# Performance work log

Measured on AMD Instinct MI355X. Metric: run time of the kernel, lower is better.

## Reference

```python
import jax, jax.numpy as jnp
import numpy as np

NUM_CLASSES = 80
INPUT_SHAPE = (416.0, 416.0)
ANCHORS_MASK0 = np.array([6, 7, 8])
CONF_THRES = 0.5
NMS_THRES = 0.4
IMAGE_SHAPE = (416.0, 416.0)
MAX_DET = 100          # fixed-size padded NMS output (jit-compatible)
CLASS_OFFSET = 4096.0  # class-aware box offset == independent per-class NMS
NEG = jnp.float32(-1e9)


def setup_inputs() -> dict:
    key = jax.random.key(0)
    inputs_1 = jax.random.normal(key, (32, 255, 52, 52), dtype=jnp.float32)
    anchors = jnp.array([[10, 13], [16, 30], [33, 23], [30, 61], [62, 45],
                         [59, 119], [116, 90], [156, 198], [373, 326]], dtype=jnp.float32)
    return {"inputs_1": inputs_1, "anchors": anchors}


def _decode(inputs_1, anchors):
    B, C, H, W = inputs_1.shape
    A = len(ANCHORS_MASK0)
    attrs = C // A  # 5 + num_classes
    # [B, A, H, W, attrs]
    pred = inputs_1.reshape(B, A, attrs, H, W).transpose(0, 1, 3, 4, 2)
    xy = jax.nn.sigmoid(pred[..., 0:2])
    wh = pred[..., 2:4]
    conf = jax.nn.sigmoid(pred[..., 4])
    cls = jax.nn.sigmoid(pred[..., 5:])
    stride_h = INPUT_SHAPE[0] / H
    stride_w = INPUT_SHAPE[1] / W
    anc = anchors[ANCHORS_MASK0] / jnp.array([stride_w, stride_h], jnp.float32)  # [A,2]
    gx = jnp.arange(W, dtype=jnp.float32)
    gy = jnp.arange(H, dtype=jnp.float32)
    bx = xy[..., 0] + gx[None, None, None, :]
    by = xy[..., 1] + gy[None, None, :, None]
    bw = jnp.exp(wh[..., 0]) * anc[:, 0][None, :, None, None]
    bh = jnp.exp(wh[..., 1]) * anc[:, 1][None, :, None, None]
    boxes = jnp.stack([bx, by, bw, bh], -1) / jnp.array([W, H, W, H], jnp.float32)
    return jnp.concatenate([boxes.reshape(B, -1, 4),
                            conf.reshape(B, -1, 1),
                            cls.reshape(B, -1, NUM_CLASSES)], axis=-1)  # [B, A*H*W, 5+C]


def _iou(box, boxes):
    lt = jnp.maximum(box[:2], boxes[:, :2])
    rb = jnp.minimum(box[2:], boxes[:, 2:])
    wh = jnp.clip(rb - lt, 0.0)
    inter = wh[:, 0] * wh[:, 1]
    a1 = (box[2] - box[0]) * (box[3] - box[1])
    a2 = (boxes[:, 2] - boxes[:, 0]) * (boxes[:, 3] - boxes[:, 1])
    return inter / (a1 + a2 - inter + 1e-9)


def _nms(pred0):
    # pred0: [N, 5+C] (image 0, matching torch code which only processes prediction[0])
    cx, cy, w, h = pred0[:, 0], pred0[:, 1], pred0[:, 2], pred0[:, 3]
    corners = jnp.stack([cx - w / 2, cy - h / 2, cx + w / 2, cy + h / 2], -1)  # [N,4]
    class_conf = jnp.max(pred0[:, 5:], axis=1)
    class_pred = jnp.argmax(pred0[:, 5:], axis=1)
    score = pred0[:, 4] * class_conf  # obj_conf * class_conf, same score nms() receives
    valid = score >= CONF_THRES
    # offsetting boxes by class id makes a single NMS pass equivalent to the per-class loop
    obox = corners + (class_pred.astype(jnp.float32) * CLASS_OFFSET)[:, None]
    s0 = jnp.where(valid, score, NEG)

    def step(scores, _):
        i = jnp.argmax(scores)
        flag = scores[i] > NEG / 2
        iou = _iou(obox[i], obox)
        new_scores = jnp.where(iou > NMS_THRES, NEG, scores).at[i].set(NEG)
        return new_scores, (i, flag)

    _, (idxs, flags) = jax.lax.scan(step, s0, None, length=MAX_DET)
    det = jnp.concatenate([
        corners[idxs],                                  # x1,y1,x2,y2
        pred0[idxs, 4:5],                               # obj conf
        class_conf[idxs][:, None],                      # class conf
        class_pred[idxs].astype(jnp.float32)[:, None],  # class id
    ], axis=1)  # [MAX_DET, 7]
    # yolo_correct_boxes: xywh -> yx min/max scaled to image_shape
    box_xy = (det[:, 0:2] + det[:, 2:4]) / 2.0
    box_wh = det[:, 2:4] - det[:, 0:2]
    box_yx = box_xy[:, ::-1]
    box_hw = box_wh[:, ::-1]
    mins = box_yx - box_hw / 2.0
    maxes = box_yx + box_hw / 2.0
    scale = jnp.array([IMAGE_SHAPE[0], IMAGE_SHAPE[1], IMAGE_SHAPE[0], IMAGE_SHAPE[1]], jnp.float32)
    boxes_corr = jnp.concatenate([mins, maxes], axis=1) * scale
    det = jnp.concatenate([boxes_corr, det[:, 4:]], axis=1)
    return det * flags[:, None].astype(jnp.float32)  # zero-padded rows where no detection


def reference(inputs_1, anchors):
    out = _decode(inputs_1, anchors)   # [B, 3*H*W, 5+num_classes]
    det = _nms(out[0])                 # [MAX_DET, 7], padded fixed-size NMS result
    return (out, det)
```

## Files before the change

kernel.cpp:

```cpp
#include <hip/hip_runtime.h>
#include <math.h>

#define NTHREADS 1024

constexpr int An = 3;
constexpr int Wd = 52;
constexpr int HWn = 2704;
constexpr int ATT = 85;
constexpr int CH = 208;
constexpr int PITCH = 209;
constexpr int CHUNKS = 13;
constexpr int BAn = 96;
constexpr int DEC_BLOCKS = BAn * CHUNKS;
constexpr int NC = An * HWn;
constexpr int NSORT = 8192;
constexpr int OUT_DEC = 32 * NC * ATT;
constexpr float NEGV = -1.0e9f;

__device__ __forceinline__ float sig_(float x) {
    return 1.0f / (1.0f + expf(-x));
}

__global__ void __launch_bounds__(NTHREADS)
yolo_fused(const float* __restrict__ in, const float* __restrict__ anc,
           float* __restrict__ out, float* __restrict__ ws)
{
    extern __shared__ float smem[];
    const int tid = threadIdx.x;

    if (blockIdx.x != 0) {
        const int bi    = (int)blockIdx.x - 1;
        const int chunk = bi % CHUNKS;
        const int ba    = bi / CHUNKS;
        const int a     = ba % An;
        const float anc_w = anc[(6 + a) * 2 + 0] * 0.125f;
        const float anc_h = anc[(6 + a) * 2 + 1] * 0.125f;
        const int pos0  = chunk * CH;
        const float* src = in + (size_t)ba * 85 * HWn + pos0;

        for (int i = tid; i < ATT * CH; i += NTHREADS) {
            const int attr = i / CH;
            const int p    = i - attr * CH;
            const int pos  = pos0 + p;
            const float x  = src[(size_t)attr * HWn + p];
            float v;
            if (attr >= 4)      v = sig_(x);
            else if (attr == 0) v = (sig_(x) + (float)(pos % Wd)) / 52.0f;
            else if (attr == 1) v = (sig_(x) + (float)(pos / Wd)) / 52.0f;
            else if (attr == 2) v = expf(x) * anc_w / 52.0f;
            else                v = expf(x) * anc_h / 52.0f;
            smem[attr * PITCH + p] = v;
        }
        __syncthreads();

        float* dst = out + ((size_t)ba * HWn + pos0) * ATT;
        for (int f = tid; f < CH * ATT; f += NTHREADS) {
            const int p    = f / ATT;
            const int attr = f - p * ATT;
            dst[f] = smem[attr * PITCH + p];
        }
        return;
    }

    float* ks       = smem;
    int*   ki       = (int*)(smem + NSORT);
    float* kept     = smem + 2 * NSORT;
    float* detstage = smem + 2 * NSORT + 416;
    int*   meta     = (int*)(smem + 2 * NSORT + 416 + 704);

    for (int i = tid; i < NSORT; i += NTHREADS) { ks[i] = NEGV; ki[i] = i; }
    if (tid == 0) meta[0] = 0;
    __syncthreads();

    for (int k = 0; k < 8; ++k) {
        const int n = tid + k * NTHREADS;
        if (n < NC) {
            const int a   = n / HWn;
            const int pos = n - a * HWn;
            const float* p = in + (size_t)a * 85 * HWn + pos;
            const float tx = p[0];
            const float ty = p[HWn];
            const float tw = p[2 * HWn];
            const float th = p[3 * HWn];
            const float tc = p[4 * HWn];
            float m = -3.0e38f; int cp = 0;
            for (int j = 0; j < 80; ++j) {
                const float x = p[(size_t)(5 + j) * HWn];
                if (x > m) { m = x; cp = j; }
            }
            const float cc    = sig_(m);
            const float conf  = sig_(tc);
            const float score = __fmul_rn(conf, cc);
            const float aw = anc[(6 + a) * 2 + 0] * 0.125f;
            const float ah = anc[(6 + a) * 2 + 1] * 0.125f;
            const float cx = (sig_(tx) + (float)(pos % Wd)) / 52.0f;
            const float cy = (sig_(ty) + (float)(pos / Wd)) / 52.0f;
            const float bw = expf(tw) * aw / 52.0f;
            const float bh = expf(th) * ah / 52.0f;
            const float hw = __fmul_rn(bw, 0.5f);
            const float hh = __fmul_rn(bh, 0.5f);
            const float x1 = __fsub_rn(cx, hw), y1 = __fsub_rn(cy, hh);
            const float x2 = __fadd_rn(cx, hw), y2 = __fadd_rn(cy, hh);
            float4* w4 = (float4*)ws;
            w4[2 * n + 0] = make_float4(x1, y1, x2, y2);
            w4[2 * n + 1] = make_float4(conf, cc, (float)cp, 0.0f);
            if (score >= 0.5f) {
                const int slot = atomicAdd(&meta[0], 1);
                ks[slot] = score;
                ki[slot] = n;
            }
        }
    }
    __threadfence_block();
    __syncthreads();
    const int V = meta[0];
    int P2 = 1; while (P2 < V) P2 <<= 1;

    for (int k = 2; k <= P2; k <<= 1) {
        for (int j = k >> 1; j > 0; j >>= 1) {
            for (int i = tid; i < P2; i += NTHREADS) {
                const int l = i ^ j;
                if (l > i) {
                    const float si = ks[i], sl = ks[l];
                    const int   ni = ki[i], nl = ki[l];
                    const bool bli = (sl > si) || (sl == si && nl < ni);
                    const bool bil = (si > sl) || (si == sl && ni < nl);
                    const bool up  = ((i & k) == 0);
                    if (up ? bli : bil) {
                        ks[i] = sl; ks[l] = si;
                        ki[i] = nl; ki[l] = ni;
                    }
                }
            }
            __syncthreads();
        }
    }

    if (tid < 64) {
        const float4* w4 = (const float4*)ws;
        float4* keptv = (float4*)kept;
        int nk = 0;

        float cx1 = 0, cy1 = 0, cx2 = 0, cy2 = 0, mconf = 0, mcc = 0, mcp = 0;
        bool act = (tid < V);
        if (act) {
            const int n = ki[tid];
            const float4 bx = w4[2 * n], mt = w4[2 * n + 1];
            cx1 = bx.x; cy1 = bx.y; cx2 = bx.z; cy2 = bx.w;
            mconf = mt.x; mcc = mt.y; mcp = mt.z;
        }

        for (int p0 = 0; p0 < V && nk < 100; p0 += 64) {
            float nx1 = 0, ny1 = 0, nx2 = 0, ny2 = 0, nco = 0, ncc = 0, ncp = 0;
            const bool actn = (p0 + 64 + tid) < V;
            if (actn) {
                const int n = ki[p0 + 64 + tid];
                const float4 bx = w4[2 * n], mt = w4[2 * n + 1];
                nx1 = bx.x; ny1 = bx.y; nx2 = bx.z; ny2 = bx.w;
                nco = mt.x; ncc = mt.y; ncp = mt.z;
            }

            const float off = __fmul_rn(mcp, 4096.0f);
            const float ox1 = __fadd_rn(cx1, off);
            const float oy1 = __fadd_rn(cy1, off);
            const float ox2 = __fadd_rn(cx2, off);
            const float oy2 = __fadd_rn(cy2, off);
            const float aC  = __fmul_rn(__fsub_rn(ox2, ox1), __fsub_rn(oy2, oy1));

            bool sup = !act;
            for (int t = 0; t < nk; ++t) {
                const float4 kb = keptv[t];
                const float ltx = fmaxf(kb.x, ox1), lty = fmaxf(kb.y, oy1);
                const float rbx = fminf(kb.z, ox2), rby = fminf(kb.w, oy2);
                const float iw = fmaxf(__fsub_rn(rbx, ltx), 0.0f);
                const float ih = fmaxf(__fsub_rn(rby, lty), 0.0f);
                const float inter = __fmul_rn(iw, ih);
                const float aK = __fmul_rn(__fsub_rn(kb.z, kb.x), __fsub_rn(kb.w, kb.y));
                const float den = __fadd_rn(__fsub_rn(__fadd_rn(aK, aC), inter), 1e-9f);
                if (inter / den > 0.4f) sup = true;
            }

            unsigned long long rem = __ballot(!sup);
            while (rem != 0ULL && nk < 100) {
                const int w = __ffsll(rem) - 1;
                const float wx1 = __shfl(ox1, w), wy1 = __shfl(oy1, w);
                const float wx2 = __shfl(ox2, w), wy2 = __shfl(oy2, w);
                const float aW  = __shfl(aC, w);
                if (tid == w) {
                    keptv[nk] = make_float4(ox1, oy1, ox2, oy2);
                    float* dr = detstage + nk * 7;
                    const float xm  = __fmul_rn(__fadd_rn(cx1, cx2), 0.5f);
                    const float ym  = __fmul_rn(__fadd_rn(cy1, cy2), 0.5f);
                    const float hw2 = __fmul_rn(__fsub_rn(cx2, cx1), 0.5f);
                    const float hh2 = __fmul_rn(__fsub_rn(cy2, cy1), 0.5f);
                    dr[0] = __fmul_rn(__fsub_rn(ym, hh2), 416.0f);
                    dr[1] = __fmul_rn(__fsub_rn(xm, hw2), 416.0f);
                    dr[2] = __fmul_rn(__fadd_rn(ym, hh2), 416.0f);
                    dr[3] = __fmul_rn(__fadd_rn(xm, hw2), 416.0f);
                    dr[4] = mconf; dr[5] = mcc; dr[6] = mcp;
                }
                ++nk;
                if (!sup && tid > w) {
                    const float ltx = fmaxf(wx1, ox1), lty = fmaxf(wy1, oy1);
                    const float rbx = fminf(wx2, ox2), rby = fminf(wy2, oy2);
                    const float iw = fmaxf(__fsub_rn(rbx, ltx), 0.0f);
                    const float ih = fmaxf(__fsub_rn(rby, lty), 0.0f);
                    const float inter = __fmul_rn(iw, ih);
                    const float den = __fadd_rn(__fsub_rn(__fadd_rn(aW, aC), inter), 1e-9f);
                    if (inter / den > 0.4f) sup = true;
                }
                rem = __ballot(!sup && tid > w);
            }

            cx1 = nx1; cy1 = ny1; cx2 = nx2; cy2 = ny2;
            mconf = nco; mcc = ncc; mcp = ncp;
            act = actn;
        }
        if (tid == 0) meta[1] = nk;
    }
    __syncthreads();

    const int nk = meta[1];
    for (int i = tid; i < 100 * 7; i += NTHREADS) {
        out[OUT_DEC + i] = (i < nk * 7) ? detstage[i] : 0.0f;
    }
}

extern "C" void kernel_launch(void* const* d_in, const int* in_sizes, int n_in,
                              void* d_out, int out_size, void* d_ws, size_t ws_size,
                              hipStream_t stream) {
    const float* in  = (const float*)d_in[0];
    const float* anc = (const float*)d_in[1];
    float* out = (float*)d_out;
    float* ws  = (float*)d_ws;
    const size_t shmem = (size_t)(ATT * PITCH) * sizeof(float);
    hipLaunchKernelGGL(yolo_fused, dim3(DEC_BLOCKS + 1), dim3(NTHREADS),
                       shmem, stream, in, anc, out, ws);
}
```

Before: 279.2 us.

## Split fused kernel into parallel prep, single-block NMS, and decode kernels

Moves per-candidate box and score preparation out of the single NMS block into a separate many-block kernel that writes boxes and scores to workspace. The NMS kernel then compacts candidates with a wave ballot and one atomic per wave, and sorts packed 64-bit score/index keys instead of separate arrays. Decode runs as its own launch after NMS. This removes the long serial prep from the single-block critical path, at the cost of extra launches and serializing NMS before decode instead of overlapping them.

```diff
diff --git a/kernel.cpp b/kernel.cpp
--- a/kernel.cpp
+++ b/kernel.cpp
@@ -1,7 +1,5 @@
 #include <hip/hip_runtime.h>
 #include <math.h>
-
-#define NTHREADS 1024
 
 constexpr int An = 3;
 constexpr int Wd = 52;
@@ -10,126 +8,111 @@
 constexpr int CH = 208;
 constexpr int PITCH = 209;
 constexpr int CHUNKS = 13;
-constexpr int BAn = 96;
-constexpr int DEC_BLOCKS = BAn * CHUNKS;
+constexpr int DEC_BLOCKS = 96 * CHUNKS;
 constexpr int NC = An * HWn;
 constexpr int NSORT = 8192;
 constexpr int OUT_DEC = 32 * NC * ATT;
 constexpr float NEGV = -1.0e9f;
+constexpr int WS_SCORE_OFF = 65536;
 
 __device__ __forceinline__ float sig_(float x) {
     return 1.0f / (1.0f + expf(-x));
 }
 
-__global__ void __launch_bounds__(NTHREADS)
-yolo_fused(const float* __restrict__ in, const float* __restrict__ anc,
-           float* __restrict__ out, float* __restrict__ ws)
+__global__ void __launch_bounds__(128)
+yolo_prep(const float* __restrict__ in, const float* __restrict__ anc,
+          float* __restrict__ ws)
 {
-    extern __shared__ float smem[];
+    const int n = blockIdx.x * 128 + threadIdx.x;
+    if (n >= NC) return;
+    const int a   = n / HWn;
+    const int pos = n - a * HWn;
+    const float* p = in + (size_t)a * 85 * HWn + pos;
+
+    const float tx = p[0];
+    const float ty = p[HWn];
+    const float tw = p[2 * HWn];
+    const float th = p[3 * HWn];
+    const float tc = p[4 * HWn];
+
+    float m = -3.0e38f; int cp = 0;
+    #pragma unroll
+    for (int j0 = 0; j0 < 80; j0 += 16) {
+        float v[16];
+        #pragma unroll
+        for (int u = 0; u < 16; ++u) v[u] = p[(size_t)(5 + j0 + u) * HWn];
+        #pragma unroll
+        for (int u = 0; u < 16; ++u) {
+            if (v[u] > m) { m = v[u]; cp = j0 + u; }
+        }
+    }
+
+    const float cc    = sig_(m);
+    const float conf  = sig_(tc);
+    const float score = __fmul_rn(conf, cc);
+    const float aw = anc[(6 + a) * 2 + 0] * 0.125f;
+    const float ah = anc[(6 + a) * 2 + 1] * 0.125f;
+    const float cx = (sig_(tx) + (float)(pos % Wd)) / 52.0f;
+    const float cy = (sig_(ty) + (float)(pos / Wd)) / 52.0f;
+    const float bw = expf(tw) * aw / 52.0f;
+    const float bh = expf(th) * ah / 52.0f;
+    const float hw = __fmul_rn(bw, 0.5f);
+    const float hh = __fmul_rn(bh, 0.5f);
+    float4* w4 = (float4*)ws;
+    w4[2 * n + 0] = make_float4(__fsub_rn(cx, hw), __fsub_rn(cy, hh),
+                                __fadd_rn(cx, hw), __fadd_rn(cy, hh));
+    w4[2 * n + 1] = make_float4(conf, cc, (float)cp, 0.0f);
+    ws[WS_SCORE_OFF + n] = score;
+}
+
+__global__ void __launch_bounds__(1024)
+yolo_nms(const float* __restrict__ ws, float* __restrict__ out)
+{
+    __shared__ unsigned long long keys[NSORT];
+    __shared__ float kept[100 * 4];
+    __shared__ float detstage[100 * 7];
+    __shared__ int   meta[2];
     const int tid = threadIdx.x;
-
-    if (blockIdx.x != 0) {
-        const int bi    = (int)blockIdx.x - 1;
-        const int chunk = bi % CHUNKS;
-        const int ba    = bi / CHUNKS;
-        const int a     = ba % An;
-        const float anc_w = anc[(6 + a) * 2 + 0] * 0.125f;
-        const float anc_h = anc[(6 + a) * 2 + 1] * 0.125f;
-        const int pos0  = chunk * CH;
-        const float* src = in + (size_t)ba * 85 * HWn + pos0;
-
-        for (int i = tid; i < ATT * CH; i += NTHREADS) {
-            const int attr = i / CH;
-            const int p    = i - attr * CH;
-            const int pos  = pos0 + p;
-            const float x  = src[(size_t)attr * HWn + p];
-            float v;
-            if (attr >= 4)      v = sig_(x);
-            else if (attr == 0) v = (sig_(x) + (float)(pos % Wd)) / 52.0f;
-            else if (attr == 1) v = (sig_(x) + (float)(pos / Wd)) / 52.0f;
-            else if (attr == 2) v = expf(x) * anc_w / 52.0f;
-            else                v = expf(x) * anc_h / 52.0f;
-            smem[attr * PITCH + p] = v;
-        }
-        __syncthreads();
-
-        float* dst = out + ((size_t)ba * HWn + pos0) * ATT;
-        for (int f = tid; f < CH * ATT; f += NTHREADS) {
-            const int p    = f / ATT;
-            const int attr = f - p * ATT;
-            dst[f] = smem[attr * PITCH + p];
-        }
-        return;
-    }
-
-    float* ks       = smem;
-    int*   ki       = (int*)(smem + NSORT);
-    float* kept     = smem + 2 * NSORT;
-    float* detstage = smem + 2 * NSORT + 416;
-    int*   meta     = (int*)(smem + 2 * NSORT + 416 + 704);
-
-    for (int i = tid; i < NSORT; i += NTHREADS) { ks[i] = NEGV; ki[i] = i; }
+    const unsigned lane = tid & 63;
+
     if (tid == 0) meta[0] = 0;
     __syncthreads();
 
+    const float* wscore = ws + WS_SCORE_OFF;
     for (int k = 0; k < 8; ++k) {
-        const int n = tid + k * NTHREADS;
-        if (n < NC) {
-            const int a   = n / HWn;
-            const int pos = n - a * HWn;
-            const float* p = in + (size_t)a * 85 * HWn + pos;
-            const float tx = p[0];
-            const float ty = p[HWn];
-            const float tw = p[2 * HWn];
-            const float th = p[3 * HWn];
-            const float tc = p[4 * HWn];
-            float m = -3.0e38f; int cp = 0;
-            for (int j = 0; j < 80; ++j) {
-                const float x = p[(size_t)(5 + j) * HWn];
-                if (x > m) { m = x; cp = j; }
-            }
-            const float cc    = sig_(m);
-            const float conf  = sig_(tc);
-            const float score = __fmul_rn(conf, cc);
-            const float aw = anc[(6 + a) * 2 + 0] * 0.125f;
-            const float ah = anc[(6 + a) * 2 + 1] * 0.125f;
-            const float cx = (sig_(tx) + (float)(pos % Wd)) / 52.0f;
-            const float cy = (sig_(ty) + (float)(pos / Wd)) / 52.0f;
-            const float bw = expf(tw) * aw / 52.0f;
-            const float bh = expf(th) * ah / 52.0f;
-            const float hw = __fmul_rn(bw, 0.5f);
-            const float hh = __fmul_rn(bh, 0.5f);
-            const float x1 = __fsub_rn(cx, hw), y1 = __fsub_rn(cy, hh);
-            const float x2 = __fadd_rn(cx, hw), y2 = __fadd_rn(cy, hh);
-            float4* w4 = (float4*)ws;
-            w4[2 * n + 0] = make_float4(x1, y1, x2, y2);
-            w4[2 * n + 1] = make_float4(conf, cc, (float)cp, 0.0f);
-            if (score >= 0.5f) {
-                const int slot = atomicAdd(&meta[0], 1);
-                ks[slot] = score;
-                ki[slot] = n;
-            }
-        }
-    }
-    __threadfence_block();
+        const int n = tid + k * 1024;
+        const float s = (n < NC) ? wscore[n] : NEGV;
+        const bool valid = (s >= 0.5f);
+        const unsigned long long mask = __ballot(valid);
+        if (mask != 0ULL) {
+            const int leader = __ffsll((long long)mask) - 1;
+            int base = 0;
+            if ((int)lane == leader) base = atomicAdd(&meta[0], __popcll(mask));
+            base = __shfl(base, leader);
+            if (valid) {
+                const int slot = base +
+                    __popcll(mask & ((1ULL << lane) - 1ULL));
+                keys[slot] =
+                    ((unsigned long long)(0xFFFFFFFFu - __float_as_uint(s)) << 32)
+                    | (unsigned)n;
+            }
+        }
+    }
     __syncthreads();
     const int V = meta[0];
     int P2 = 1; while (P2 < V) P2 <<= 1;
 
+    for (int i = V + tid; i < P2; i += 1024) keys[i] = ~0ULL;
+    __syncthreads();
+
     for (int k = 2; k <= P2; k <<= 1) {
         for (int j = k >> 1; j > 0; j >>= 1) {
-            for (int i = tid; i < P2; i += NTHREADS) {
+            for (int i = tid; i < P2; i += 1024) {
                 const int l = i ^ j;
                 if (l > i) {
-                    const float si = ks[i], sl = ks[l];
-                    const int   ni = ki[i], nl = ki[l];
-                    const bool bli = (sl > si) || (sl == si && nl < ni);
-                    const bool bil = (si > sl) || (si == sl && ni < nl);
-                    const bool up  = ((i & k) == 0);
-                    if (up ? bli : bil) {
-                        ks[i] = sl; ks[l] = si;
-                        ki[i] = nl; ki[l] = ni;
-                    }
+                    const unsigned long long a = keys[i], b = keys[l];
+                    const bool up = ((i & k) == 0);
+                    if (up ? (b < a) : (a < b)) { keys[i] = b; keys[l] = a; }
                 }
             }
             __syncthreads();
@@ -144,7 +127,7 @@
         float cx1 = 0, cy1 = 0, cx2 = 0, cy2 = 0, mconf = 0, mcc = 0, mcp = 0;
         bool act = (tid < V);
         if (act) {
-            const int n = ki[tid];
+            const int n = (int)(keys[tid] & 0xFFFFFFFFu);
             const float4 bx = w4[2 * n], mt = w4[2 * n + 1];
             cx1 = bx.x; cy1 = bx.y; cx2 = bx.z; cy2 = bx.w;
             mconf = mt.x; mcc = mt.y; mcp = mt.z;
@@ -154,7 +137,7 @@
             float nx1 = 0, ny1 = 0, nx2 = 0, ny2 = 0, nco = 0, ncc = 0, ncp = 0;
             const bool actn = (p0 + 64 + tid) < V;
             if (actn) {
-                const int n = ki[p0 + 64 + tid];
+                const int n = (int)(keys[p0 + 64 + tid] & 0xFFFFFFFFu);
                 const float4 bx = w4[2 * n], mt = w4[2 * n + 1];
                 nx1 = bx.x; ny1 = bx.y; nx2 = bx.z; ny2 = bx.w;
                 nco = mt.x; ncc = mt.y; ncp = mt.z;
@@ -182,7 +165,7 @@
 
             unsigned long long rem = __ballot(!sup);
             while (rem != 0ULL && nk < 100) {
-                const int w = __ffsll(rem) - 1;
+                const int w = __ffsll((long long)rem) - 1;
                 const float wx1 = __shfl(ox1, w), wy1 = __shfl(oy1, w);
                 const float wx2 = __shfl(ox2, w), wy2 = __shfl(oy2, w);
                 const float aW  = __shfl(aC, w);
@@ -221,8 +204,46 @@
     __syncthreads();
 
     const int nk = meta[1];
-    for (int i = tid; i < 100 * 7; i += NTHREADS) {
+    for (int i = tid; i < 100 * 7; i += 1024) {
         out[OUT_DEC + i] = (i < nk * 7) ? detstage[i] : 0.0f;
+    }
+}
+
+__global__ void __launch_bounds__(1024)
+yolo_decode(const float* __restrict__ in, const float* __restrict__ anc,
+            float* __restrict__ out)
+{
+    extern __shared__ float smem[];
+    const int tid = threadIdx.x;
+    const int bi    = (int)blockIdx.x;
+    const int chunk = bi % CHUNKS;
+    const int ba    = bi / CHUNKS;
+    const int a     = ba % An;
+    const float anc_w = anc[(6 + a) * 2 + 0] * 0.125f;
+    const float anc_h = anc[(6 + a) * 2 + 1] * 0.125f;
+    const int pos0  = chunk * CH;
+    const float* src = in + (size_t)ba * 85 * HWn + pos0;
+
+    for (int i = tid; i < ATT * CH; i += 1024) {
+        const int attr = i / CH;
+        const int p    = i - attr * CH;
+        const int pos  = pos0 + p;
+        const float x  = src[(size_t)attr * HWn + p];
+        float v;
+        if (attr >= 4)      v = sig_(x);
+        else if (attr == 0) v = (sig_(x) + (float)(pos % Wd)) / 52.0f;
+        else if (attr == 1) v = (sig_(x) + (float)(pos / Wd)) / 52.0f;
+        else if (attr == 2) v = expf(x) * anc_w / 52.0f;
+        else                v = expf(x) * anc_h / 52.0f;
+        smem[attr * PITCH + p] = v;
+    }
+    __syncthreads();
+
+    float* dst = out + ((size_t)ba * HWn + pos0) * ATT;
+    for (int f = tid; f < CH * ATT; f += 1024) {
+        const int p    = f / ATT;
+        const int attr = f - p * ATT;
+        dst[f] = smem[attr * PITCH + p];
     }
 }
 
@@ -233,7 +254,11 @@
     const float* anc = (const float*)d_in[1];
     float* out = (float*)d_out;
     float* ws  = (float*)d_ws;
+
+    hipLaunchKernelGGL(yolo_prep, dim3((NC + 127) / 128), dim3(128), 0, stream,
+                       in, anc, ws);
+    hipLaunchKernelGGL(yolo_nms, dim3(1), dim3(1024), 0, stream, ws, out);
     const size_t shmem = (size_t)(ATT * PITCH) * sizeof(float);
-    hipLaunchKernelGGL(yolo_fused, dim3(DEC_BLOCKS + 1), dim3(NTHREADS),
-                       shmem, stream, in, anc, out, ws);
-}
+    hipLaunchKernelGGL(yolo_decode, dim3(DEC_BLOCKS), dim3(1024), shmem, stream,
+                       in, anc, out);
+}
```

After: 273.7 us. Within noise of the previous version (-1.9%).
